# Optimization experiments

Measured on AMD Instinct MI355X. Metric: run time of the kernel, lower is better.

## Reference

```python
import jax, jax.numpy as jnp
import numpy as np

B, S, H = 8, 2048, 1024
NEG = -1e10


def setup_inputs() -> dict:
    key = jax.random.key(0)
    ks = jax.random.split(key, 8)
    scale = 1.0 / np.sqrt(H)
    return {
        "x": jax.random.normal(ks[0], (B, S, H), dtype=jnp.float32),
        "pad_mask": jax.random.randint(ks[1], (B, S), 0, 2, dtype=jnp.int32),
        "Wq": jax.random.uniform(ks[2], (H, H), jnp.float32, -scale, scale),
        "bq": jax.random.uniform(ks[3], (H,), jnp.float32, -scale, scale),
        "Wk": jax.random.uniform(ks[4], (H, H), jnp.float32, -scale, scale),
        "bk": jax.random.uniform(ks[5], (H,), jnp.float32, -scale, scale),
        "Wv": jax.random.uniform(ks[6], (H, H), jnp.float32, -scale, scale),
        "bv": jax.random.uniform(ks[7], (H,), jnp.float32, -scale, scale),
    }


def reference(x, pad_mask, Wq, bq, Wk, bk, Wv, bv):
    # Linear projections (torch Linear: x @ W.T + b)
    q = x @ Wq.T + bq  # [B,S,H]
    k = x @ Wk.T + bk
    v = x @ Wv.T + bv
    weight = jnp.einsum("bid,bjd->bij", q, k)  # [B,S,S]
    seq = x.shape[1]
    # causal mask (strictly upper triangular) + padding mask over key positions
    causal = jnp.triu(jnp.ones((seq, seq), dtype=jnp.float32), k=1)  # [S,S]
    pad = pad_mask.astype(jnp.float32)[:, None, :]  # [B,1,S] -> key axis
    mask = (causal[None, :, :] + pad) > 0  # [B,S,S]
    # torch code fills BEFORE scaling; replicate exactly
    weight = jnp.where(mask, NEG, weight)
    score = jax.nn.softmax(weight / jnp.sqrt(jnp.float32(weight.shape[-1] * 0 + x.shape[-1])), axis=-1)
    return jnp.einsum("bij,bjd->bid", score, v)
```

## Files before the change

### kernel.cpp

```cpp
#include <hip/hip_runtime.h>

typedef __attribute__((ext_vector_type(8))) short short8;
typedef __attribute__((ext_vector_type(4))) short short4v;
typedef __attribute__((ext_vector_type(4))) float float4v;

typedef const __attribute__((address_space(1))) unsigned int* gptr_t;
typedef __attribute__((address_space(3))) unsigned int* lptr_t;

__device__ __forceinline__ unsigned short f2bf(float f) {
  unsigned u = __float_as_uint(f);
  u += 0x7FFFu + ((u >> 16) & 1u);
  return (unsigned short)(u >> 16);
}
__device__ __forceinline__ float bf2f(unsigned short h) {
  return __uint_as_float(((unsigned)h) << 16);
}

__global__ __launch_bounds__(256) void cvtW_kernel(const float* __restrict__ Wq,
                                                   const float* __restrict__ Wk,
                                                   const float* __restrict__ Wv,
                                                   unsigned short* __restrict__ wb) {
  int blk = blockIdx.x;
  int r = blk >> 10;
  const float* src = (r == 0) ? Wq : ((r == 1) ? Wk : Wv);
  int t = threadIdx.x;
  int i = (blk & 1023) * 256 + t;
  float4v v = ((const float4v*)src)[i];
  short4v o;
  o[0] = (short)f2bf(v[0]);
  o[1] = (short)f2bf(v[1]);
  o[2] = (short)f2bf(v[2]);
  o[3] = (short)f2bf(v[3]);
  ((short4v*)(wb + (size_t)r * 1048576u))[i] = o;
}

__global__ __launch_bounds__(256) void compact_kernel(const int* __restrict__ pad,
                                                      int* __restrict__ jmap,
                                                      int* __restrict__ cntb,
                                                      float* __restrict__ mean_x) {
  int b = blockIdx.x;
  const int* prow = pad + b * 2048;
  int t = threadIdx.x;
  float4v z = {0.f, 0.f, 0.f, 0.f};
  ((float4v*)(mean_x + b * 1024))[t] = z;
  int base = t * 8;
  int ind[8], incl[8];
  int s = 0;
#pragma unroll
  for (int e = 0; e < 8; ++e) {
    ind[e] = (prow[base + e] == 0);
    s += ind[e];
    incl[e] = s;
  }
  int lane = t & 63, wv = t >> 6;
  int v = s;
#pragma unroll
  for (int off = 1; off < 64; off <<= 1) {
    int u = __shfl_up(v, off);
    if (lane >= off) v += u;
  }
  __shared__ int wsum[4];
  if (lane == 63) wsum[wv] = v;
  __syncthreads();
  int wbase = 0;
  for (int w = 0; w < wv; ++w) wbase += wsum[w];
  int excl_base = wbase + v - s;
#pragma unroll
  for (int e = 0; e < 8; ++e) {
    int cnt_i = excl_base + incl[e];
    cntb[b * 2048 + base + e] = cnt_i;
    if (ind[e]) jmap[b * 2048 + cnt_i - 1] = base + e;
  }
}

__global__ __launch_bounds__(256) void prep_kernel(const float* __restrict__ x,
                                                   const int* __restrict__ pad,
                                                   const int* __restrict__ cntb,
                                                   unsigned short* __restrict__ xb,
                                                   unsigned short* __restrict__ xc) {
  int i = blockIdx.x, b = blockIdx.y;
  int idx = b * 2048 + i;
  int t = threadIdx.x;
  float4v v = ((const float4v*)(x + (size_t)idx * 1024))[t];
  short4v o;
  o[0] = (short)f2bf(v[0]);
  o[1] = (short)f2bf(v[1]);
  o[2] = (short)f2bf(v[2]);
  o[3] = (short)f2bf(v[3]);
  ((short4v*)(xb + (size_t)idx * 1024))[t] = o;
  if (pad[idx] == 0) {
    int jc = cntb[idx] - 1;
    ((short4v*)(xc + ((size_t)(b * 2048 + jc)) * 1024))[t] = o;
  }
}

__global__ __launch_bounds__(256) void zerofillX_kernel(const int* __restrict__ cntb,
                                                        unsigned short* __restrict__ xc) {
  int b = blockIdx.y;
  int Nc = cntb[b * 2048 + 2047];
  int W = (Nc + 127) & ~127;
  int jc = Nc + blockIdx.x;
  if (jc >= W) return;
  short4v z = {0, 0, 0, 0};
  ((short4v*)(xc + ((size_t)(b * 2048 + jc)) * 1024))[threadIdx.x] = z;
}

__global__ __launch_bounds__(256) void meanx_kernel(const unsigned short* __restrict__ xb,
                                                    float* __restrict__ mean_x) {
  int b = blockIdx.x, hblk = blockIdx.y, iblk = blockIdx.z;
  int h = hblk * 256 + threadIdx.x;
  float s = 0.f;
  const unsigned short* base = xb + ((size_t)b * 2048 + (size_t)iblk * 256) * 1024 + h;
  for (int i = 0; i < 256; ++i) s += bf2f(base[(size_t)i * 1024]);
  atomicAdd(&mean_x[b * 1024 + h], s);
}

__global__ __launch_bounds__(256) void gemv_kernel(const float* __restrict__ mean_x,
                                                   const unsigned short* __restrict__ wv,
                                                   const float* __restrict__ bv,
                                                   float* __restrict__ fixmean) {
  int b = blockIdx.x, dblk = blockIdx.y;
  int d = dblk * 256 + threadIdx.x;
  const unsigned short* wrow = wv + (size_t)d * 1024;
  const float* mx = mean_x + b * 1024;
  float s = 0.f;
  for (int h = 0; h < 1024; h += 8) {
    short8 w = *(const short8*)(wrow + h);
#pragma unroll
    for (int e = 0; e < 8; ++e) s += mx[h + e] * bf2f(((const unsigned short*)&w)[e]);
  }
  fixmean[b * 1024 + d] = s * (1.0f / 2048.0f) + bv[d];
}

template <int MODE>
__global__ __launch_bounds__(256, 4) void gemm_bt_kernel(
    const unsigned short* __restrict__ A, const unsigned short* __restrict__ A2,
    const unsigned short* __restrict__ B,
    const float* __restrict__ b1, const float* __restrict__ b2, const float* __restrict__ b3,
    void* __restrict__ C, unsigned short* __restrict__ C2, unsigned short* __restrict__ C3,
    const int* __restrict__ cnt,
    int K, int lda, int ldb, int ldc, size_t sA, size_t sB, size_t sC) {
  constexpr int BN = (MODE == 0) ? 128 : 64;
  constexpr int BCH = (MODE == 0) ? 4 : 2;
  constexpr int MI = (MODE == 0) ? 4 : 2;

  int bx = blockIdx.x, by = blockIdx.y, bz = blockIdx.z;
  const unsigned short* Aptr = A;
  if (MODE == 0) {
    int wg = by * 24 + bx;
    int s = (wg & 7) * 384 + (wg >> 3);
    bx = s % 24;
    by = s / 24;
    int r = bx >> 3;
    if (r > 0) {
      int b = by >> 4;
      if (((by & 15) << 7) >= cnt[(b << 11) + 2047]) return;
      Aptr = A2;
    }
  }
  int Kend = K;
  if (MODE == 1) {
    int tc = cnt[(bz << 11) + (by * 128 + 127)];
    if (bx * 64 >= tc) return;
  }
  if (MODE == 2) {
    int tc = cnt[(bz << 11) + (by * 128 + 127)];
    Kend = (tc + 63) & ~63;
  }

  __shared__ __align__(16) char lds[16384 + BN * 128];
  char* ldsA = lds;
  char* ldsB = lds + 16384;

  int tid = threadIdx.x;
  int wave = tid >> 6, lane = tid & 63;
  int lm = lane & 15, g = lane >> 4;
  int wm = wave >> 1, wn = wave & 1;
  int swl = (lm & 7) << 4;

  float4v acc[MI][4];
#pragma unroll
  for (int i = 0; i < MI; ++i)
#pragma unroll
    for (int j = 0; j < 4; ++j) {
      float4v z = {0.f, 0.f, 0.f, 0.f};
      acc[i][j] = z;
    }

  const char* Abase = (const char*)(Aptr + sA * (size_t)bz + (size_t)(by * 128) * (size_t)lda);
  const char* Bbase = (const char*)(B + sB * (size_t)bz + (size_t)(bx * BN) * (size_t)ldb);
  size_t strideA = (size_t)lda * 2u;
  size_t strideB = (size_t)ldb * 2u;

  int Lbase = wave * 1024 + lane * 16;

  for (int kt = 0; kt < Kend; kt += 64) {
#pragma unroll
    for (int c = 0; c < 4; ++c) {
      int L = c * 4096 + Lbase;
      int row = L >> 7;
      int lb = (L & 127) ^ ((row & 7) << 4);
      const char* ga = Abase + (size_t)row * strideA + (size_t)(kt * 2) + lb;
      __builtin_amdgcn_global_load_lds((gptr_t)(const void*)ga,
                                       (lptr_t)(void*)(ldsA + c * 4096 + wave * 1024), 16, 0, 0);
    }
#pragma unroll
    for (int c = 0; c < BCH; ++c) {
      int L = c * 4096 + Lbase;
      int row = L >> 7;
      int lb = (L & 127) ^ ((row & 7) << 4);
      const char* gb = Bbase + (size_t)row * strideB + (size_t)(kt * 2) + lb;
      __builtin_amdgcn_global_load_lds((gptr_t)(const void*)gb,
                                       (lptr_t)(void*)(ldsB + c * 4096 + wave * 1024), 16, 0, 0);
    }
    __syncthreads();

#pragma unroll
    for (int k0 = 0; k0 < 64; k0 += 32) {
      short8 af[MI], bfv[4];
      int b0 = (k0 * 2 + 16 * g) ^ swl;
#pragma unroll
      for (int mi = 0; mi < MI; ++mi) {
        int ra = (MODE == 0 ? wm * 64 : wave * 32) + mi * 16 + lm;
        af[mi] = *(const short8*)(ldsA + ra * 128 + b0);
      }
#pragma unroll
      for (int ni = 0; ni < 4; ++ni) {
        int rb = (MODE == 0 ? wn * 64 : 0) + ni * 16 + lm;
        bfv[ni] = *(const short8*)(ldsB + rb * 128 + b0);
      }
#pragma unroll
      for (int mi = 0; mi < MI; ++mi)
#pragma unroll
        for (int ni = 0; ni < 4; ++ni)
          acc[mi][ni] =
              __builtin_amdgcn_mfma_f32_16x16x32_bf16(af[mi], bfv[ni], acc[mi][ni], 0, 0, 0);
    }
    __syncthreads();
  }

  int mb = by * 128 + (MODE == 0 ? wm * 64 : wave * 32) + g * 4;
  int nb = bx * BN + (MODE == 0 ? wn * 64 : 0) + lm;
#pragma unroll
  for (int mi = 0; mi < MI; ++mi) {
#pragma unroll
    for (int ni = 0; ni < 4; ++ni) {
      int n = nb + ni * 16;
      float bias = 0.0f;
      if (MODE == 0) {
        int nn = n & 1023;
        int r = n >> 10;
        bias = (r == 0) ? b1[nn] : ((r == 1) ? b2[nn] : b3[nn]);
      }
#pragma unroll
      for (int r4 = 0; r4 < 4; ++r4) {
        int m = mb + mi * 16 + r4;
        float v = acc[mi][ni][r4] + bias;
        if (MODE == 0) {
          int nn = n & 1023;
          int r = n >> 10;
          if (r == 0) {
            ((unsigned short*)C)[(size_t)m * 1024u + nn] = f2bf(v);
          } else if (r == 1) {
            C3[(size_t)m * 1024u + nn] = f2bf(v);
          } else {
            size_t idx = ((size_t)(m >> 11) << 21) + ((size_t)nn << 11) + (size_t)(m & 2047);
            C2[idx] = f2bf(v);
          }
        } else if (MODE == 1) {
          ((unsigned short*)C)[sC * (size_t)bz + (size_t)m * (size_t)ldc + n] = f2bf(v);
        } else {
          ((float*)C)[sC * (size_t)bz + (size_t)m * (size_t)ldc + n] = v;
        }
      }
    }
  }
}

__global__ __launch_bounds__(256) void softmax_kernel(unsigned short* __restrict__ sp,
                                                      const int* __restrict__ cntb) {
  int i = blockIdx.x, b = blockIdx.y;
  int cnt_i = cntb[b * 2048 + i];
  int tcnt = cntb[b * 2048 + (i | 127)];
  int W = (tcnt + 63) & ~63;
  unsigned short* row = sp + ((size_t)b * 2048 + (size_t)i) * 2048;
  int tid = threadIdx.x;
  int j0 = tid * 8;
  bool active = (j0 < W);

  float t[8];
  if (active) {
    short8 sv = *(const short8*)(row + j0);
#pragma unroll
    for (int e = 0; e < 8; ++e) {
      int jc = j0 + e;
      bool msk = (jc >= cnt_i);
      float raw = bf2f(((const unsigned short*)&sv)[e]);
      t[e] = (msk ? -1e10f : raw) * 0.03125f;
    }
  } else {
#pragma unroll
    for (int e = 0; e < 8; ++e) t[e] = -1e10f * 0.03125f;
  }

  float m = t[0];
#pragma unroll
  for (int e = 1; e < 8; ++e) m = fmaxf(m, t[e]);
#pragma unroll
  for (int o = 32; o > 0; o >>= 1) m = fmaxf(m, __shfl_xor(m, o));
  __shared__ float redm[4], reds[4];
  int wv = tid >> 6, ln = tid & 63;
  if (ln == 0) redm[wv] = m;
  __syncthreads();
  m = fmaxf(fmaxf(redm[0], redm[1]), fmaxf(redm[2], redm[3]));

  float p[8];
  float s = 0.f;
#pragma unroll
  for (int e = 0; e < 8; ++e) {
    p[e] = __expf(t[e] - m);
    s += p[e];
  }
#pragma unroll
  for (int o = 32; o > 0; o >>= 1) s += __shfl_xor(s, o);
  if (ln == 0) reds[wv] = s;
  __syncthreads();
  s = reds[0] + reds[1] + reds[2] + reds[3];
  float inv = 1.0f / s;

  if (active) {
    short8 ov;
#pragma unroll
    for (int e = 0; e < 8; ++e) ((unsigned short*)&ov)[e] = (short)f2bf(p[e] * inv);
    *(short8*)(row + j0) = ov;
  }
}

__global__ __launch_bounds__(256) void fixup_apply_kernel(const int* __restrict__ cntb,
                                                          const float* __restrict__ fixmean,
                                                          float* __restrict__ out) {
  int b = blockIdx.x, dchunk = blockIdx.y;
  int d = dchunk * 256 + threadIdx.x;
  float val = fixmean[b * 1024 + d];
  for (int i = 0; i < 2048; ++i) {
    if (cntb[b * 2048 + i] != 0) break;
    out[((size_t)b * 2048 + (size_t)i) * 1024 + d] = val;
  }
}

extern "C" void kernel_launch(void* const* d_in, const int* in_sizes, int n_in,
                              void* d_out, int out_size, void* d_ws, size_t ws_size,
                              hipStream_t stream) {
  const float* x = (const float*)d_in[0];
  const int* pad = (const int*)d_in[1];
  const float* Wq = (const float*)d_in[2];
  const float* bq = (const float*)d_in[3];
  const float* Wk = (const float*)d_in[4];
  const float* bk = (const float*)d_in[5];
  const float* Wv = (const float*)d_in[6];
  const float* bv = (const float*)d_in[7];
  float* out = (float*)d_out;

  char* ws = (char*)d_ws;
  unsigned short* xb  = (unsigned short*)(ws + 0);
  unsigned short* xc  = (unsigned short*)(ws + 33554432);
  unsigned short* wb  = (unsigned short*)(ws + 67108864);
  int*   jmap    = (int*)(ws + 73400320);
  int*   cntb    = (int*)(ws + 73465856);
  float* mean_x  = (float*)(ws + 73531392);
  float* fixmean = (float*)(ws + 73564160);
  unsigned short* qb  = (unsigned short*)(ws + 75497472);
  unsigned short* vtc = (unsigned short*)(ws + 109051904);
  unsigned short* sp  = (unsigned short*)(ws + 142606336);
  unsigned short* kcb = (unsigned short*)(ws + 209715200);

  compact_kernel<<<8, 256, 0, stream>>>(pad, jmap, cntb, mean_x);

  cvtW_kernel<<<3072, 256, 0, stream>>>(Wq, Wk, Wv, wb);
  dim3 gp(2048, 8);
  prep_kernel<<<gp, 256, 0, stream>>>(x, pad, cntb, xb, xc);
  dim3 gz(128, 8);
  zerofillX_kernel<<<gz, 256, 0, stream>>>(cntb, xc);
  dim3 gmx(8, 4, 8);
  meanx_kernel<<<gmx, 256, 0, stream>>>(xb, mean_x);

  dim3 g1(24, 128, 1);
  gemm_bt_kernel<0><<<g1, 256, 0, stream>>>(xb, xc, wb, bq, bk, bv, qb, vtc, kcb, cntb,
                                            1024, 1024, 1024, 1024, 0, 0, 0);

  dim3 g3(8, 4);
  gemv_kernel<<<g3, 256, 0, stream>>>(mean_x, wb + 2097152, bv, fixmean);

  dim3 g4(32, 16, 8);
  gemm_bt_kernel<1><<<g4, 256, 0, stream>>>(qb, nullptr, kcb, nullptr, nullptr, nullptr,
                                            sp, nullptr, nullptr, cntb,
                                            1024, 1024, 1024, 2048, 2097152, 2097152, 4194304);

  dim3 g5(2048, 8);
  softmax_kernel<<<g5, 256, 0, stream>>>(sp, cntb);

  dim3 g6(16, 16, 8);
  gemm_bt_kernel<2><<<g6, 256, 0, stream>>>(sp, nullptr, vtc, nullptr, nullptr, nullptr,
                                            out, nullptr, nullptr, cntb,
                                            2048, 2048, 2048, 1024, 4194304, 2097152, 2097152);

  fixup_apply_kernel<<<g3, 256, 0, stream>>>(cntb, fixmean, out);
}
```

Measured before the change: 308.1 us.

## Replace GEMM with 4-stage LDS pipeline and uniform 128x128 tiles

```diff
diff --git a/kernel.cpp b/kernel.cpp
--- a/kernel.cpp
+++ b/kernel.cpp
@@ -133,17 +133,13 @@
 }
 
 template <int MODE>
-__global__ __launch_bounds__(256, 4) void gemm_bt_kernel(
+__global__ __launch_bounds__(256, 2) void gemm_deep_kernel(
     const unsigned short* __restrict__ A, const unsigned short* __restrict__ A2,
     const unsigned short* __restrict__ B,
     const float* __restrict__ b1, const float* __restrict__ b2, const float* __restrict__ b3,
     void* __restrict__ C, unsigned short* __restrict__ C2, unsigned short* __restrict__ C3,
     const int* __restrict__ cnt,
     int K, int lda, int ldb, int ldc, size_t sA, size_t sB, size_t sC) {
-  constexpr int BN = (MODE == 0) ? 128 : 64;
-  constexpr int BCH = (MODE == 0) ? 4 : 2;
-  constexpr int MI = (MODE == 0) ? 4 : 2;
-
   int bx = blockIdx.x, by = blockIdx.y, bz = blockIdx.z;
   const unsigned short* Aptr = A;
   if (MODE == 0) {
@@ -161,16 +157,15 @@
   int Kend = K;
   if (MODE == 1) {
     int tc = cnt[(bz << 11) + (by * 128 + 127)];
-    if (bx * 64 >= tc) return;
+    if (bx * 128 >= tc) return;
   }
   if (MODE == 2) {
     int tc = cnt[(bz << 11) + (by * 128 + 127)];
     Kend = (tc + 63) & ~63;
   }
-
-  __shared__ __align__(16) char lds[16384 + BN * 128];
-  char* ldsA = lds;
-  char* ldsB = lds + 16384;
+  int nt = Kend >> 5;
+
+  __shared__ __align__(16) char lds[65536];
 
   int tid = threadIdx.x;
   int wave = tid >> 6, lane = tid & 63;
@@ -178,9 +173,9 @@
   int wm = wave >> 1, wn = wave & 1;
   int swl = (lm & 7) << 4;
 
-  float4v acc[MI][4];
-#pragma unroll
-  for (int i = 0; i < MI; ++i)
+  float4v acc[4][4];
+#pragma unroll
+  for (int i = 0; i < 4; ++i)
 #pragma unroll
     for (int j = 0; j < 4; ++j) {
       float4v z = {0.f, 0.f, 0.f, 0.f};
@@ -188,61 +183,73 @@
     }
 
   const char* Abase = (const char*)(Aptr + sA * (size_t)bz + (size_t)(by * 128) * (size_t)lda);
-  const char* Bbase = (const char*)(B + sB * (size_t)bz + (size_t)(bx * BN) * (size_t)ldb);
+  const char* Bbase = (const char*)(B + sB * (size_t)bz + (size_t)(bx * 128) * (size_t)ldb);
   size_t strideA = (size_t)lda * 2u;
   size_t strideB = (size_t)ldb * 2u;
 
   int Lbase = wave * 1024 + lane * 16;
 
-  for (int kt = 0; kt < Kend; kt += 64) {
-#pragma unroll
-    for (int c = 0; c < 4; ++c) {
+  auto STAGE = [&](int t) {
+    char* slot = lds + (t & 3) * 16384;
+    int kbyte = t * 64;
+#pragma unroll
+    for (int c = 0; c < 2; ++c) {
       int L = c * 4096 + Lbase;
-      int row = L >> 7;
-      int lb = (L & 127) ^ ((row & 7) << 4);
-      const char* ga = Abase + (size_t)row * strideA + (size_t)(kt * 2) + lb;
+      int rp = L >> 7;
+      int un = (L & 127) ^ ((rp & 7) << 4);
+      int grow = rp + ((un >> 6) << 6);
+      int gb = un & 63;
+      const char* ga = Abase + (size_t)grow * strideA + kbyte + gb;
       __builtin_amdgcn_global_load_lds((gptr_t)(const void*)ga,
-                                       (lptr_t)(void*)(ldsA + c * 4096 + wave * 1024), 16, 0, 0);
+                                       (lptr_t)(void*)(slot + L), 16, 0, 0);
+      const char* gbp = Bbase + (size_t)grow * strideB + kbyte + gb;
+      __builtin_amdgcn_global_load_lds((gptr_t)(const void*)gbp,
+                                       (lptr_t)(void*)(slot + 8192 + L), 16, 0, 0);
     }
-#pragma unroll
-    for (int c = 0; c < BCH; ++c) {
-      int L = c * 4096 + Lbase;
-      int row = L >> 7;
-      int lb = (L & 127) ^ ((row & 7) << 4);
-      const char* gb = Bbase + (size_t)row * strideB + (size_t)(kt * 2) + lb;
-      __builtin_amdgcn_global_load_lds((gptr_t)(const void*)gb,
-                                       (lptr_t)(void*)(ldsB + c * 4096 + wave * 1024), 16, 0, 0);
-    }
-    __syncthreads();
-
-#pragma unroll
-    for (int k0 = 0; k0 < 64; k0 += 32) {
-      short8 af[MI], bfv[4];
-      int b0 = (k0 * 2 + 16 * g) ^ swl;
-#pragma unroll
-      for (int mi = 0; mi < MI; ++mi) {
-        int ra = (MODE == 0 ? wm * 64 : wave * 32) + mi * 16 + lm;
-        af[mi] = *(const short8*)(ldsA + ra * 128 + b0);
-      }
-#pragma unroll
-      for (int ni = 0; ni < 4; ++ni) {
-        int rb = (MODE == 0 ? wn * 64 : 0) + ni * 16 + lm;
-        bfv[ni] = *(const short8*)(ldsB + rb * 128 + b0);
-      }
-#pragma unroll
-      for (int mi = 0; mi < MI; ++mi)
-#pragma unroll
-        for (int ni = 0; ni < 4; ++ni)
-          acc[mi][ni] =
-              __builtin_amdgcn_mfma_f32_16x16x32_bf16(af[mi], bfv[ni], acc[mi][ni], 0, 0, 0);
-    }
-    __syncthreads();
-  }
-
-  int mb = by * 128 + (MODE == 0 ? wm * 64 : wave * 32) + g * 4;
-  int nb = bx * BN + (MODE == 0 ? wn * 64 : 0) + lm;
-#pragma unroll
-  for (int mi = 0; mi < MI; ++mi) {
+  };
+
+  if (nt > 0) STAGE(0);
+  if (nt > 1) STAGE(1);
+  if (nt > 2) STAGE(2);
+
+  int birA = ((wm << 6) | (g << 4)) ^ swl;
+  int birB = ((wn << 6) | (g << 4)) ^ swl;
+
+  for (int t = 0; t < nt; ++t) {
+    int rem = nt - 1 - t;
+    if (rem >= 2)
+      asm volatile("s_waitcnt vmcnt(8)" ::: "memory");
+    else if (rem == 1)
+      asm volatile("s_waitcnt vmcnt(4)" ::: "memory");
+    else
+      asm volatile("s_waitcnt vmcnt(0)" ::: "memory");
+    asm volatile("s_barrier" ::: "memory");
+    if (t + 3 < nt) STAGE(t + 3);
+
+    const char* Ab = lds + (t & 3) * 16384;
+    const char* Bb = Ab + 8192;
+    short8 af[4], bfv[4];
+#pragma unroll
+    for (int mi = 0; mi < 4; ++mi)
+      af[mi] = *(const short8*)(Ab + (mi * 16 + lm) * 128 + birA);
+#pragma unroll
+    for (int ni = 0; ni < 4; ++ni)
+      bfv[ni] = *(const short8*)(Bb + (ni * 16 + lm) * 128 + birB);
+
+    __builtin_amdgcn_s_setprio(1);
+#pragma unroll
+    for (int mi = 0; mi < 4; ++mi)
+#pragma unroll
+      for (int ni = 0; ni < 4; ++ni)
+        acc[mi][ni] =
+            __builtin_amdgcn_mfma_f32_16x16x32_bf16(af[mi], bfv[ni], acc[mi][ni], 0, 0, 0);
+    __builtin_amdgcn_s_setprio(0);
+  }
+
+  int mb = by * 128 + wm * 64 + g * 4;
+  int nb = bx * 128 + wn * 64 + lm;
+#pragma unroll
+  for (int mi = 0; mi < 4; ++mi) {
 #pragma unroll
     for (int ni = 0; ni < 4; ++ni) {
       int n = nb + ni * 16;
@@ -385,24 +392,24 @@
   meanx_kernel<<<gmx, 256, 0, stream>>>(xb, mean_x);
 
   dim3 g1(24, 128, 1);
-  gemm_bt_kernel<0><<<g1, 256, 0, stream>>>(xb, xc, wb, bq, bk, bv, qb, vtc, kcb, cntb,
-                                            1024, 1024, 1024, 1024, 0, 0, 0);
+  gemm_deep_kernel<0><<<g1, 256, 0, stream>>>(xb, xc, wb, bq, bk, bv, qb, vtc, kcb, cntb,
+                                              1024, 1024, 1024, 1024, 0, 0, 0);
 
   dim3 g3(8, 4);
   gemv_kernel<<<g3, 256, 0, stream>>>(mean_x, wb + 2097152, bv, fixmean);
 
-  dim3 g4(32, 16, 8);
-  gemm_bt_kernel<1><<<g4, 256, 0, stream>>>(qb, nullptr, kcb, nullptr, nullptr, nullptr,
-                                            sp, nullptr, nullptr, cntb,
-                                            1024, 1024, 1024, 2048, 2097152, 2097152, 4194304);
+  dim3 g4(16, 16, 8);
+  gemm_deep_kernel<1><<<g4, 256, 0, stream>>>(qb, nullptr, kcb, nullptr, nullptr, nullptr,
+                                              sp, nullptr, nullptr, cntb,
+                                              1024, 1024, 1024, 2048, 2097152, 2097152, 4194304);
 
   dim3 g5(2048, 8);
   softmax_kernel<<<g5, 256, 0, stream>>>(sp, cntb);
 
-  dim3 g6(16, 16, 8);
-  gemm_bt_kernel<2><<<g6, 256, 0, stream>>>(sp, nullptr, vtc, nullptr, nullptr, nullptr,
-                                            out, nullptr, nullptr, cntb,
-                                            2048, 2048, 2048, 1024, 4194304, 2097152, 2097152);
+  dim3 g6(8, 16, 8);
+  gemm_deep_kernel<2><<<g6, 256, 0, stream>>>(sp, nullptr, vtc, nullptr, nullptr, nullptr,
+                                              out, nullptr, nullptr, cntb,
+                                              2048, 2048, 2048, 1024, 4194304, 2097152, 2097152);
 
   fixup_apply_kernel<<<g3, 256, 0, stream>>>(cntb, fixmean, out);
 }
```

Result: slower. 322.2 us (+4.6%).

## Split GEMM kernels and use 128x128 tiles with 512 threads for attention GEMMs

Applied to the files above, without the earlier changes.

```diff
diff --git a/kernel.cpp b/kernel.cpp
--- a/kernel.cpp
+++ b/kernel.cpp
@@ -107,12 +107,22 @@
 
 __global__ __launch_bounds__(256) void meanx_kernel(const unsigned short* __restrict__ xb,
                                                     float* __restrict__ mean_x) {
-  int b = blockIdx.x, hblk = blockIdx.y, iblk = blockIdx.z;
-  int h = hblk * 256 + threadIdx.x;
-  float s = 0.f;
-  const unsigned short* base = xb + ((size_t)b * 2048 + (size_t)iblk * 256) * 1024 + h;
-  for (int i = 0; i < 256; ++i) s += bf2f(base[(size_t)i * 1024]);
-  atomicAdd(&mean_x[b * 1024 + h], s);
+  int iblk = blockIdx.x, b = blockIdx.y;
+  int t = threadIdx.x;
+  const unsigned short* base = xb + ((size_t)b * 2048 + (size_t)iblk * 64) * 1024 + t * 4;
+  float s0 = 0.f, s1 = 0.f, s2 = 0.f, s3 = 0.f;
+  for (int r = 0; r < 64; ++r) {
+    short4v v = *(const short4v*)(base + (size_t)r * 1024);
+    s0 += bf2f(((const unsigned short*)&v)[0]);
+    s1 += bf2f(((const unsigned short*)&v)[1]);
+    s2 += bf2f(((const unsigned short*)&v)[2]);
+    s3 += bf2f(((const unsigned short*)&v)[3]);
+  }
+  float* mp = mean_x + b * 1024 + t * 4;
+  atomicAdd(mp + 0, s0);
+  atomicAdd(mp + 1, s1);
+  atomicAdd(mp + 2, s2);
+  atomicAdd(mp + 3, s3);
 }
 
 __global__ __launch_bounds__(256) void gemv_kernel(const float* __restrict__ mean_x,
@@ -132,43 +142,26 @@
   fixmean[b * 1024 + d] = s * (1.0f / 2048.0f) + bv[d];
 }
 
-template <int MODE>
-__global__ __launch_bounds__(256, 4) void gemm_bt_kernel(
+__global__ __launch_bounds__(256, 4) void gemm_proj_kernel(
     const unsigned short* __restrict__ A, const unsigned short* __restrict__ A2,
     const unsigned short* __restrict__ B,
     const float* __restrict__ b1, const float* __restrict__ b2, const float* __restrict__ b3,
-    void* __restrict__ C, unsigned short* __restrict__ C2, unsigned short* __restrict__ C3,
-    const int* __restrict__ cnt,
-    int K, int lda, int ldb, int ldc, size_t sA, size_t sB, size_t sC) {
-  constexpr int BN = (MODE == 0) ? 128 : 64;
-  constexpr int BCH = (MODE == 0) ? 4 : 2;
-  constexpr int MI = (MODE == 0) ? 4 : 2;
-
-  int bx = blockIdx.x, by = blockIdx.y, bz = blockIdx.z;
+    unsigned short* __restrict__ C, unsigned short* __restrict__ C2,
+    unsigned short* __restrict__ C3, const int* __restrict__ cnt) {
+  int bx = blockIdx.x, by = blockIdx.y;
+  int wg = by * 24 + bx;
+  int s = (wg & 7) * 384 + (wg >> 3);
+  bx = s % 24;
+  by = s / 24;
   const unsigned short* Aptr = A;
-  if (MODE == 0) {
-    int wg = by * 24 + bx;
-    int s = (wg & 7) * 384 + (wg >> 3);
-    bx = s % 24;
-    by = s / 24;
-    int r = bx >> 3;
-    if (r > 0) {
-      int b = by >> 4;
-      if (((by & 15) << 7) >= cnt[(b << 11) + 2047]) return;
-      Aptr = A2;
-    }
-  }
-  int Kend = K;
-  if (MODE == 1) {
-    int tc = cnt[(bz << 11) + (by * 128 + 127)];
-    if (bx * 64 >= tc) return;
-  }
-  if (MODE == 2) {
-    int tc = cnt[(bz << 11) + (by * 128 + 127)];
-    Kend = (tc + 63) & ~63;
-  }
-
-  __shared__ __align__(16) char lds[16384 + BN * 128];
+  int r = bx >> 3;
+  if (r > 0) {
+    int b = by >> 4;
+    if (((by & 15) << 7) >= cnt[(b << 11) + 2047]) return;
+    Aptr = A2;
+  }
+
+  __shared__ __align__(16) char lds[32768];
   char* ldsA = lds;
   char* ldsB = lds + 16384;
 
@@ -178,23 +171,23 @@
   int wm = wave >> 1, wn = wave & 1;
   int swl = (lm & 7) << 4;
 
-  float4v acc[MI][4];
-#pragma unroll
-  for (int i = 0; i < MI; ++i)
+  float4v acc[4][4];
+#pragma unroll
+  for (int i = 0; i < 4; ++i)
 #pragma unroll
     for (int j = 0; j < 4; ++j) {
       float4v z = {0.f, 0.f, 0.f, 0.f};
       acc[i][j] = z;
     }
 
-  const char* Abase = (const char*)(Aptr + sA * (size_t)bz + (size_t)(by * 128) * (size_t)lda);
-  const char* Bbase = (const char*)(B + sB * (size_t)bz + (size_t)(bx * BN) * (size_t)ldb);
-  size_t strideA = (size_t)lda * 2u;
-  size_t strideB = (size_t)ldb * 2u;
+  const char* Abase = (const char*)(Aptr + (size_t)(by * 128) * 1024u);
+  const char* Bbase = (const char*)(B + (size_t)(bx * 128) * 1024u);
+  size_t strideA = 2048u;
+  size_t strideB = 2048u;
 
   int Lbase = wave * 1024 + lane * 16;
 
-  for (int kt = 0; kt < Kend; kt += 64) {
+  for (int kt = 0; kt < 1024; kt += 64) {
 #pragma unroll
     for (int c = 0; c < 4; ++c) {
       int L = c * 4096 + Lbase;
@@ -203,12 +196,6 @@
       const char* ga = Abase + (size_t)row * strideA + (size_t)(kt * 2) + lb;
       __builtin_amdgcn_global_load_lds((gptr_t)(const void*)ga,
                                        (lptr_t)(void*)(ldsA + c * 4096 + wave * 1024), 16, 0, 0);
-    }
-#pragma unroll
-    for (int c = 0; c < BCH; ++c) {
-      int L = c * 4096 + Lbase;
-      int row = L >> 7;
-      int lb = (L & 127) ^ ((row & 7) << 4);
       const char* gb = Bbase + (size_t)row * strideB + (size_t)(kt * 2) + lb;
       __builtin_amdgcn_global_load_lds((gptr_t)(const void*)gb,
                                        (lptr_t)(void*)(ldsB + c * 4096 + wave * 1024), 16, 0, 0);
@@ -217,20 +204,20 @@
 
 #pragma unroll
     for (int k0 = 0; k0 < 64; k0 += 32) {
-      short8 af[MI], bfv[4];
+      short8 af[4], bfv[4];
       int b0 = (k0 * 2 + 16 * g) ^ swl;
 #pragma unroll
-      for (int mi = 0; mi < MI; ++mi) {
-        int ra = (MODE == 0 ? wm * 64 : wave * 32) + mi * 16 + lm;
-        af[mi] = *(const short8*)(ldsA + ra * 128 + b0);
+      for (int mi = 0; mi < 4; ++mi) {
+        const char* p = ldsA + (wm * 64 + mi * 16 + lm) * 128;
+        af[mi] = *(const short8*)(p + b0);
       }
 #pragma unroll
       for (int ni = 0; ni < 4; ++ni) {
-        int rb = (MODE == 0 ? wn * 64 : 0) + ni * 16 + lm;
-        bfv[ni] = *(const short8*)(ldsB + rb * 128 + b0);
-      }
-#pragma unroll
-      for (int mi = 0; mi < MI; ++mi)
+        const char* p = ldsB + (wn * 64 + ni * 16 + lm) * 128;
+        bfv[ni] = *(const short8*)(p + b0);
+      }
+#pragma unroll
+      for (int mi = 0; mi < 4; ++mi)
 #pragma unroll
         for (int ni = 0; ni < 4; ++ni)
           acc[mi][ni] =
@@ -239,35 +226,124 @@
     __syncthreads();
   }
 
-  int mb = by * 128 + (MODE == 0 ? wm * 64 : wave * 32) + g * 4;
-  int nb = bx * BN + (MODE == 0 ? wn * 64 : 0) + lm;
-#pragma unroll
-  for (int mi = 0; mi < MI; ++mi) {
+  int mb = by * 128 + wm * 64 + g * 4;
+  int nb = bx * 128 + wn * 64 + lm;
+#pragma unroll
+  for (int mi = 0; mi < 4; ++mi) {
 #pragma unroll
     for (int ni = 0; ni < 4; ++ni) {
       int n = nb + ni * 16;
-      float bias = 0.0f;
-      if (MODE == 0) {
-        int nn = n & 1023;
-        int r = n >> 10;
-        bias = (r == 0) ? b1[nn] : ((r == 1) ? b2[nn] : b3[nn]);
-      }
+      int nn = n & 1023;
+      int rr = n >> 10;
+      float bias = (rr == 0) ? b1[nn] : ((rr == 1) ? b2[nn] : b3[nn]);
 #pragma unroll
       for (int r4 = 0; r4 < 4; ++r4) {
         int m = mb + mi * 16 + r4;
         float v = acc[mi][ni][r4] + bias;
-        if (MODE == 0) {
-          int nn = n & 1023;
-          int r = n >> 10;
-          if (r == 0) {
-            ((unsigned short*)C)[(size_t)m * 1024u + nn] = f2bf(v);
-          } else if (r == 1) {
-            C3[(size_t)m * 1024u + nn] = f2bf(v);
-          } else {
-            size_t idx = ((size_t)(m >> 11) << 21) + ((size_t)nn << 11) + (size_t)(m & 2047);
-            C2[idx] = f2bf(v);
-          }
-        } else if (MODE == 1) {
+        if (rr == 0) {
+          C[(size_t)m * 1024u + nn] = f2bf(v);
+        } else if (rr == 1) {
+          C3[(size_t)m * 1024u + nn] = f2bf(v);
+        } else {
+          size_t idx = ((size_t)(m >> 11) << 21) + ((size_t)nn << 11) + (size_t)(m & 2047);
+          C2[idx] = f2bf(v);
+        }
+      }
+    }
+  }
+}
+
+template <int MODE>
+__global__ __launch_bounds__(512, 8) void gemm_att_kernel(
+    const unsigned short* __restrict__ A, const unsigned short* __restrict__ B,
+    void* __restrict__ C, const int* __restrict__ cnt,
+    int K, int lda, int ldb, int ldc, size_t sA, size_t sB, size_t sC) {
+  int bx = blockIdx.x, by = blockIdx.y, bz = blockIdx.z;
+  int Kend = K;
+  int tc = cnt[(bz << 11) + (by * 128 + 127)];
+  if (MODE == 1) {
+    if (bx * 128 >= tc) return;
+  } else {
+    Kend = (tc + 63) & ~63;
+  }
+
+  __shared__ __align__(16) char lds[32768];
+  char* ldsA = lds;
+  char* ldsB = lds + 16384;
+
+  int tid = threadIdx.x;
+  int wave = tid >> 6, lane = tid & 63;
+  int lm = lane & 15, g = lane >> 4;
+  int wm = wave & 3, wn = wave >> 2;
+  int swl = (lm & 7) << 4;
+
+  float4v acc[2][4];
+#pragma unroll
+  for (int i = 0; i < 2; ++i)
+#pragma unroll
+    for (int j = 0; j < 4; ++j) {
+      float4v z = {0.f, 0.f, 0.f, 0.f};
+      acc[i][j] = z;
+    }
+
+  const char* Abase = (const char*)(A + sA * (size_t)bz + (size_t)(by * 128) * (size_t)lda);
+  const char* Bbase = (const char*)(B + sB * (size_t)bz + (size_t)(bx * 128) * (size_t)ldb);
+  size_t strideA = (size_t)lda * 2u;
+  size_t strideB = (size_t)ldb * 2u;
+
+  int Lbase = tid * 16;
+
+  for (int kt = 0; kt < Kend; kt += 64) {
+#pragma unroll
+    for (int c = 0; c < 2; ++c) {
+      int L = c * 8192 + Lbase;
+      int row = L >> 7;
+      int lb = (L & 127) ^ ((row & 7) << 4);
+      const char* ga = Abase + (size_t)row * strideA + (size_t)(kt * 2) + lb;
+      __builtin_amdgcn_global_load_lds((gptr_t)(const void*)ga,
+                                       (lptr_t)(void*)(ldsA + L), 16, 0, 0);
+      const char* gb = Bbase + (size_t)row * strideB + (size_t)(kt * 2) + lb;
+      __builtin_amdgcn_global_load_lds((gptr_t)(const void*)gb,
+                                       (lptr_t)(void*)(ldsB + L), 16, 0, 0);
+    }
+    __syncthreads();
+
+#pragma unroll
+    for (int k0 = 0; k0 < 64; k0 += 32) {
+      short8 af[2], bfv[4];
+      int b0 = (k0 * 2 + 16 * g) ^ swl;
+#pragma unroll
+      for (int mi = 0; mi < 2; ++mi) {
+        const char* p = ldsA + (wm * 32 + mi * 16 + lm) * 128;
+        af[mi] = *(const short8*)(p + b0);
+      }
+#pragma unroll
+      for (int ni = 0; ni < 4; ++ni) {
+        const char* p = ldsB + (wn * 64 + ni * 16 + lm) * 128;
+        bfv[ni] = *(const short8*)(p + b0);
+      }
+#pragma unroll
+      for (int mi = 0; mi < 2; ++mi)
+#pragma unroll
+        for (int ni = 0; ni < 4; ++ni)
+          acc[mi][ni] =
+              __builtin_amdgcn_mfma_f32_16x16x32_bf16(af[mi], bfv[ni], acc[mi][ni], 0, 0, 0);
+    }
+    __syncthreads();
+  }
+
+  int mb = by * 128 + wm * 32 + g * 4;
+  int nb = bx * 128 + wn * 64 + lm;
+#pragma unroll
+  for (int mi = 0; mi < 2; ++mi) {
+#pragma unroll
+    for (int ni = 0; ni < 4; ++ni) {
+      int n = nb + ni * 16;
+#pragma unroll
+      for (int r4 = 0; r4 < 4; ++r4) {
+        int m = mb + mi * 16 + r4;
+        float v = acc[mi][ni][r4];
+        if (MODE == 1) {
           ((unsigned short*)C)[sC * (size_t)bz + (size_t)m * (size_t)ldc + n] = f2bf(v);
         } else {
           ((float*)C)[sC * (size_t)bz + (size_t)m * (size_t)ldc + n] = v;
@@ -381,28 +457,27 @@
   prep_kernel<<<gp, 256, 0, stream>>>(x, pad, cntb, xb, xc);
   dim3 gz(128, 8);
   zerofillX_kernel<<<gz, 256, 0, stream>>>(cntb, xc);
-  dim3 gmx(8, 4, 8);
+  dim3 gmx(32, 8);
   meanx_kernel<<<gmx, 256, 0, stream>>>(xb, mean_x);
 
   dim3 g1(24, 128, 1);
-  gemm_bt_kernel<0><<<g1, 256, 0, stream>>>(xb, xc, wb, bq, bk, bv, qb, vtc, kcb, cntb,
-                                            1024, 1024, 1024, 1024, 0, 0, 0);
+  gemm_proj_kernel<<<g1, 256, 0, stream>>>(xb, xc, wb, bq, bk, bv, qb, vtc, kcb, cntb);
 
   dim3 g3(8, 4);
   gemv_kernel<<<g3, 256, 0, stream>>>(mean_x, wb + 2097152, bv, fixmean);
 
-  dim3 g4(32, 16, 8);
-  gemm_bt_kernel<1><<<g4, 256, 0, stream>>>(qb, nullptr, kcb, nullptr, nullptr, nullptr,
-                                            sp, nullptr, nullptr, cntb,
-                                            1024, 1024, 1024, 2048, 2097152, 2097152, 4194304);
+  dim3 g4(16, 16, 8);
+  gemm_att_kernel<1><<<g4, 512, 0, stream>>>(qb, kcb, sp, cntb,
+                                             1024, 1024, 1024, 2048,
+                                             2097152, 2097152, 4194304);
 
   dim3 g5(2048, 8);
   softmax_kernel<<<g5, 256, 0, stream>>>(sp, cntb);
 
-  dim3 g6(16, 16, 8);
-  gemm_bt_kernel<2><<<g6, 256, 0, stream>>>(sp, nullptr, vtc, nullptr, nullptr, nullptr,
-                                            out, nullptr, nullptr, cntb,
-                                            2048, 2048, 2048, 1024, 4194304, 2097152, 2097152);
+  dim3 g6(8, 16, 8);
+  gemm_att_kernel<2><<<g6, 512, 0, stream>>>(sp, vtc, out, cntb,
+                                             2048, 2048, 2048, 1024,
+                                             4194304, 2097152, 2097152);
 
   fixup_apply_kernel<<<g3, 256, 0, stream>>>(cntb, fixmean, out);
 }
```

Result: slower. 324.4 us (+5.3%).

## Use 128x128 tiles for all GEMMs, fold zero-fill into prep, vectorize meanx

Applied to the files above, without the earlier changes.

```diff
diff --git a/kernel.cpp b/kernel.cpp
--- a/kernel.cpp
+++ b/kernel.cpp
@@ -92,27 +92,31 @@
     int jc = cntb[idx] - 1;
     ((short4v*)(xc + ((size_t)(b * 2048 + jc)) * 1024))[t] = o;
   }
-}
-
-__global__ __launch_bounds__(256) void zerofillX_kernel(const int* __restrict__ cntb,
-                                                        unsigned short* __restrict__ xc) {
-  int b = blockIdx.y;
   int Nc = cntb[b * 2048 + 2047];
-  int W = (Nc + 127) & ~127;
-  int jc = Nc + blockIdx.x;
-  if (jc >= W) return;
-  short4v z = {0, 0, 0, 0};
-  ((short4v*)(xc + ((size_t)(b * 2048 + jc)) * 1024))[threadIdx.x] = z;
+  if (i >= Nc && i < ((Nc + 127) & ~127)) {
+    short4v z = {0, 0, 0, 0};
+    ((short4v*)(xc + ((size_t)(b * 2048 + i)) * 1024))[t] = z;
+  }
 }
 
 __global__ __launch_bounds__(256) void meanx_kernel(const unsigned short* __restrict__ xb,
                                                     float* __restrict__ mean_x) {
-  int b = blockIdx.x, hblk = blockIdx.y, iblk = blockIdx.z;
-  int h = hblk * 256 + threadIdx.x;
-  float s = 0.f;
-  const unsigned short* base = xb + ((size_t)b * 2048 + (size_t)iblk * 256) * 1024 + h;
-  for (int i = 0; i < 256; ++i) s += bf2f(base[(size_t)i * 1024]);
-  atomicAdd(&mean_x[b * 1024 + h], s);
+  int iblk = blockIdx.x, b = blockIdx.y;
+  int t = threadIdx.x;
+  const unsigned short* base = xb + ((size_t)b * 2048 + (size_t)iblk * 64) * 1024 + t * 4;
+  float s0 = 0.f, s1 = 0.f, s2 = 0.f, s3 = 0.f;
+  for (int r = 0; r < 64; ++r) {
+    short4v v = *(const short4v*)(base + (size_t)r * 1024);
+    s0 += bf2f(((const unsigned short*)&v)[0]);
+    s1 += bf2f(((const unsigned short*)&v)[1]);
+    s2 += bf2f(((const unsigned short*)&v)[2]);
+    s3 += bf2f(((const unsigned short*)&v)[3]);
+  }
+  float* mp = mean_x + b * 1024 + t * 4;
+  atomicAdd(mp + 0, s0);
+  atomicAdd(mp + 1, s1);
+  atomicAdd(mp + 2, s2);
+  atomicAdd(mp + 3, s3);
 }
 
 __global__ __launch_bounds__(256) void gemv_kernel(const float* __restrict__ mean_x,
@@ -133,17 +137,13 @@
 }
 
 template <int MODE>
-__global__ __launch_bounds__(256, 4) void gemm_bt_kernel(
+__global__ __launch_bounds__(256, 5) void gemm_bt_kernel(
     const unsigned short* __restrict__ A, const unsigned short* __restrict__ A2,
     const unsigned short* __restrict__ B,
     const float* __restrict__ b1, const float* __restrict__ b2, const float* __restrict__ b3,
     void* __restrict__ C, unsigned short* __restrict__ C2, unsigned short* __restrict__ C3,
     const int* __restrict__ cnt,
     int K, int lda, int ldb, int ldc, size_t sA, size_t sB, size_t sC) {
-  constexpr int BN = (MODE == 0) ? 128 : 64;
-  constexpr int BCH = (MODE == 0) ? 4 : 2;
-  constexpr int MI = (MODE == 0) ? 4 : 2;
-
   int bx = blockIdx.x, by = blockIdx.y, bz = blockIdx.z;
   const unsigned short* Aptr = A;
   if (MODE == 0) {
@@ -161,14 +161,14 @@
   int Kend = K;
   if (MODE == 1) {
     int tc = cnt[(bz << 11) + (by * 128 + 127)];
-    if (bx * 64 >= tc) return;
+    if (bx * 128 >= tc) return;
   }
   if (MODE == 2) {
     int tc = cnt[(bz << 11) + (by * 128 + 127)];
     Kend = (tc + 63) & ~63;
   }
 
-  __shared__ __align__(16) char lds[16384 + BN * 128];
+  __shared__ __align__(16) char lds[32768];
   char* ldsA = lds;
   char* ldsB = lds + 16384;
 
@@ -178,9 +178,9 @@
   int wm = wave >> 1, wn = wave & 1;
   int swl = (lm & 7) << 4;
 
-  float4v acc[MI][4];
-#pragma unroll
-  for (int i = 0; i < MI; ++i)
+  float4v acc[4][4];
+#pragma unroll
+  for (int i = 0; i < 4; ++i)
 #pragma unroll
     for (int j = 0; j < 4; ++j) {
       float4v z = {0.f, 0.f, 0.f, 0.f};
@@ -188,7 +188,7 @@
     }
 
   const char* Abase = (const char*)(Aptr + sA * (size_t)bz + (size_t)(by * 128) * (size_t)lda);
-  const char* Bbase = (const char*)(B + sB * (size_t)bz + (size_t)(bx * BN) * (size_t)ldb);
+  const char* Bbase = (const char*)(B + sB * (size_t)bz + (size_t)(bx * 128) * (size_t)ldb);
   size_t strideA = (size_t)lda * 2u;
   size_t strideB = (size_t)ldb * 2u;
 
@@ -203,12 +203,6 @@
       const char* ga = Abase + (size_t)row * strideA + (size_t)(kt * 2) + lb;
       __builtin_amdgcn_global_load_lds((gptr_t)(const void*)ga,
                                        (lptr_t)(void*)(ldsA + c * 4096 + wave * 1024), 16, 0, 0);
-    }
-#pragma unroll
-    for (int c = 0; c < BCH; ++c) {
-      int L = c * 4096 + Lbase;
-      int row = L >> 7;
-      int lb = (L & 127) ^ ((row & 7) << 4);
       const char* gb = Bbase + (size_t)row * strideB + (size_t)(kt * 2) + lb;
       __builtin_amdgcn_global_load_lds((gptr_t)(const void*)gb,
                                        (lptr_t)(void*)(ldsB + c * 4096 + wave * 1024), 16, 0, 0);
@@ -217,20 +211,20 @@
 
 #pragma unroll
     for (int k0 = 0; k0 < 64; k0 += 32) {
-      short8 af[MI], bfv[4];
+      short8 af[4], bfv[4];
       int b0 = (k0 * 2 + 16 * g) ^ swl;
 #pragma unroll
-      for (int mi = 0; mi < MI; ++mi) {
-        int ra = (MODE == 0 ? wm * 64 : wave * 32) + mi * 16 + lm;
-        af[mi] = *(const short8*)(ldsA + ra * 128 + b0);
+      for (int mi = 0; mi < 4; ++mi) {
+        const char* p = ldsA + (wm * 64 + mi * 16 + lm) * 128;
+        af[mi] = *(const short8*)(p + b0);
       }
 #pragma unroll
       for (int ni = 0; ni < 4; ++ni) {
-        int rb = (MODE == 0 ? wn * 64 : 0) + ni * 16 + lm;
-        bfv[ni] = *(const short8*)(ldsB + rb * 128 + b0);
+        const char* p = ldsB + (wn * 64 + ni * 16 + lm) * 128;
+        bfv[ni] = *(const short8*)(p + b0);
       }
 #pragma unroll
-      for (int mi = 0; mi < MI; ++mi)
+      for (int mi = 0; mi < 4; ++mi)
 #pragma unroll
         for (int ni = 0; ni < 4; ++ni)
           acc[mi][ni] =
@@ -239,10 +233,10 @@
     __syncthreads();
   }
 
-  int mb = by * 128 + (MODE == 0 ? wm * 64 : wave * 32) + g * 4;
-  int nb = bx * BN + (MODE == 0 ? wn * 64 : 0) + lm;
-#pragma unroll
-  for (int mi = 0; mi < MI; ++mi) {
+  int mb = by * 128 + wm * 64 + g * 4;
+  int nb = bx * 128 + wn * 64 + lm;
+#pragma unroll
+  for (int mi = 0; mi < 4; ++mi) {
 #pragma unroll
     for (int ni = 0; ni < 4; ++ni) {
       int n = nb + ni * 16;
@@ -379,9 +373,7 @@
   cvtW_kernel<<<3072, 256, 0, stream>>>(Wq, Wk, Wv, wb);
   dim3 gp(2048, 8);
   prep_kernel<<<gp, 256, 0, stream>>>(x, pad, cntb, xb, xc);
-  dim3 gz(128, 8);
-  zerofillX_kernel<<<gz, 256, 0, stream>>>(cntb, xc);
-  dim3 gmx(8, 4, 8);
+  dim3 gmx(32, 8);
   meanx_kernel<<<gmx, 256, 0, stream>>>(xb, mean_x);
 
   dim3 g1(24, 128, 1);
@@ -391,7 +383,7 @@
   dim3 g3(8, 4);
   gemv_kernel<<<g3, 256, 0, stream>>>(mean_x, wb + 2097152, bv, fixmean);
 
-  dim3 g4(32, 16, 8);
+  dim3 g4(16, 16, 8);
   gemm_bt_kernel<1><<<g4, 256, 0, stream>>>(qb, nullptr, kcb, nullptr, nullptr, nullptr,
                                             sp, nullptr, nullptr, cntb,
                                             1024, 1024, 1024, 2048, 2097152, 2097152, 4194304);
@@ -399,7 +391,7 @@
   dim3 g5(2048, 8);
   softmax_kernel<<<g5, 256, 0, stream>>>(sp, cntb);
 
-  dim3 g6(16, 16, 8);
+  dim3 g6(8, 16, 8);
   gemm_bt_kernel<2><<<g6, 256, 0, stream>>>(sp, nullptr, vtc, nullptr, nullptr, nullptr,
                                             out, nullptr, nullptr, cntb,
                                             2048, 2048, 2048, 1024, 4194304, 2097152, 2097152);
```

New measurement: 427.1 us. 1.39x slower.
